# Optimization experiments

Measured on AMD Instinct MI355X. Metric: run time of the kernel, lower is better.

## Reference

```python
import jax, jax.numpy as jnp
import numpy as np

RADIUS = 1.3
RES = 256
N_INT = 128
STEP = 0.02


def grid_sample3d(grid, coords):
    # grid: [C, D, H, W]; coords: [N, 3] as (x, y, z) in [-1, 1]
    # trilinear, align_corners=True, border clamp (torch grid_sample semantics)
    D, H, W = grid.shape[1], grid.shape[2], grid.shape[3]

    def to_idx(c, size):
        return jnp.clip((c + 1.0) * 0.5 * (size - 1), 0.0, size - 1.0)

    x = to_idx(coords[:, 0], W)
    y = to_idx(coords[:, 1], H)
    z = to_idx(coords[:, 2], D)
    x0 = jnp.floor(x).astype(jnp.int32)
    y0 = jnp.floor(y).astype(jnp.int32)
    z0 = jnp.floor(z).astype(jnp.int32)
    x1 = jnp.minimum(x0 + 1, W - 1)
    y1 = jnp.minimum(y0 + 1, H - 1)
    z1 = jnp.minimum(z0 + 1, D - 1)
    wx = x - x0.astype(x.dtype)
    wy = y - y0.astype(y.dtype)
    wz = z - z0.astype(z.dtype)

    def g(zi, yi, xi):
        return grid[:, zi, yi, xi]  # [C, N]

    c00 = g(z0, y0, x0) * (1 - wx) + g(z0, y0, x1) * wx
    c01 = g(z0, y1, x0) * (1 - wx) + g(z0, y1, x1) * wx
    c10 = g(z1, y0, x0) * (1 - wx) + g(z1, y0, x1) * wx
    c11 = g(z1, y1, x0) * (1 - wx) + g(z1, y1, x1) * wx
    c0 = c00 * (1 - wy) + c01 * wy
    c1 = c10 * (1 - wy) + c11 * wy
    return (c0 * (1 - wz) + c1 * wz).T  # [N, C]


def sh16(d):
    # real spherical harmonics, degree 4 (instant-ngp / tcnn convention), d unit
    x, y, z = d[:, 0], d[:, 1], d[:, 2]
    xx, yy, zz = x * x, y * y, z * z
    xy, yz, xz = x * y, y * z, x * z
    return jnp.stack([
        jnp.full_like(x, 0.28209479177387814),
        -0.48860251190291987 * y,
        0.48860251190291987 * z,
        -0.48860251190291987 * x,
        1.0925484305920792 * xy,
        -1.0925484305920792 * yz,
        0.94617469575755997 * zz - 0.31539156525251999,
        -1.0925484305920792 * xz,
        0.54627421529603959 * (xx - yy),
        0.59004358992664352 * y * (-3.0 * xx + yy),
        2.8906114426405538 * xy * z,
        0.45704579946446572 * y * (1.0 - 5.0 * zz),
        0.3731763325901154 * z * (5.0 * zz - 3.0),
        0.45704579946446572 * x * (1.0 - 5.0 * zz),
        1.445305721320277 * z * (xx - yy),
        0.59004358992664352 * x * (-xx + 3.0 * yy),
    ], axis=-1)  # [N, 16]


def mlp3(x, W0, W1, W2):
    # FullyFusedMLP: no bias, ReLU hidden, linear output
    h = jnp.maximum(x @ W0, 0.0)
    h = jnp.maximum(h @ W1, 0.0)
    return h @ W2


def setup_inputs() -> dict:
    key = jax.random.key(0)
    k = jax.random.split(key, 10)
    B, FD, NF = 4096, 32, 16
    rays_o = jax.random.normal(k[0], (B, 3), jnp.float32) * 0.5
    rays_d = jax.random.normal(k[1], (B, 3), jnp.float32)
    G1 = jax.random.normal(k[2], (3, RES, RES, RES), jnp.float32) * 0.02
    F = jax.random.normal(k[3], (FD, NF, NF, NF), jnp.float32) * 0.05
    W_sig0 = jax.random.normal(k[4], (FD, 128), jnp.float32) / np.sqrt(FD).astype(np.float32)
    W_sig1 = jax.random.normal(k[5], (128, 128), jnp.float32) / np.float32(np.sqrt(128))
    W_sig2 = jax.random.normal(k[6], (128, 16), jnp.float32) / np.float32(np.sqrt(128))
    W_col0 = jax.random.normal(k[7], (31, 64), jnp.float32) / np.float32(np.sqrt(31))
    W_col1 = jax.random.normal(k[8], (64, 64), jnp.float32) / np.float32(np.sqrt(64))
    W_col2 = jax.random.normal(k[9], (64, 3), jnp.float32) / np.float32(np.sqrt(64))
    return {"rays_o": rays_o, "rays_d": rays_d, "G1": G1, "F": F,
            "W_sig0": W_sig0, "W_sig1": W_sig1, "W_sig2": W_sig2,
            "W_col0": W_col0, "W_col1": W_col1, "W_col2": W_col2}


def reference(rays_o, rays_d, G1, F, W_sig0, W_sig1, W_sig2, W_col0, W_col1, W_col2):
    B = rays_o.shape[0]
    d = rays_d / jnp.linalg.norm(rays_d, axis=-1, keepdims=True)
    # ray-sphere intersection |o + t d| = RADIUS (unit d)
    b = jnp.sum(rays_o * d, axis=-1)
    c = jnp.sum(rays_o * rays_o, axis=-1) - RADIUS ** 2
    disc = b * b - c
    hit = disc > 0
    s = jnp.sqrt(jnp.where(hit, disc, 1.0))
    tmin = jnp.where(hit, jnp.maximum(-b - s, 0.0), 0.0)
    tmax = jnp.where(hit, -b + s, 0.0)
    t = tmin[:, None] + jnp.arange(N_INT + 1, dtype=jnp.float32)[None, :] * STEP  # [B, n+1]
    tmid = 0.5 * (t[:, :-1] + t[:, 1:])  # [B, n]
    mask = hit[:, None] & (tmid <= tmax[:, None])  # [B, n]
    pts = rays_o[:, None, :] + d[:, None, :] * tmid[..., None]  # [B, n, 3]
    coords = (pts / RADIUS).reshape(-1, 3)  # in [-1, 1]
    # hash/indirection lookup: G1 gives learned coords into feature grid F
    g1 = grid_sample3d(G1, coords)        # [N, 3]
    feats = grid_sample3d(F, g1)          # [N, 32]
    sig_out = mlp3(feats, W_sig0, W_sig1, W_sig2)  # [N, 16]
    sigma = jnp.where(mask, sig_out[:, 0].reshape(B, N_INT), 0.0)
    sigma = jnp.maximum(sigma, 0.0)
    pd = jnp.broadcast_to(d[:, None, :], (B, N_INT, 3)).reshape(-1, 3)
    enc = sh16(pd)
    col_raw = mlp3(jnp.concatenate([enc, sig_out[:, 1:]], axis=-1), W_col0, W_col1, W_col2)
    col = jnp.where(mask[..., None], col_raw.reshape(B, N_INT, 3), 0.0)
    # volume rendering (sigma2alpha + shrgb2rgb with white background)
    alpha = 1.0 - jnp.exp(-sigma * STEP)
    T = jnp.cumprod(1.0 - alpha + 1e-10, axis=1)
    T_excl = jnp.concatenate([jnp.ones((B, 1), alpha.dtype), T[:, :-1]], axis=1)
    w = alpha * T_excl
    rgb = jnp.einsum('bn,bnc->bc', w, jax.nn.sigmoid(col))
    rgb = rgb + (1.0 - jnp.sum(w, axis=1, keepdims=True))
    return rgb
```

## Files before the change

kernel.cpp:

```cpp
#include <hip/hip_runtime.h>
#include <stdint.h>

#define STEP 0.02f
#define INV_RADIUS (1.0f/1.3f)
#define RADIUS 1.3f

typedef __bf16 bf16x8 __attribute__((ext_vector_type(8)));
typedef float  f32x4  __attribute__((ext_vector_type(4)));

#define FT_OFF   0
#define W0_OFF   262144
#define W1_OFF   270336
#define W2_OFF   303104
#define C0_OFF   307200
#define C1_OFF   311296
#define C2_OFF   319488

#define FE_OFF    0
#define HA_OFF    4096
#define HB_OFF    8192
#define CIN_OFF   12288
#define SIG_OFF   13312
#define COL_OFF   13824
#define WAVE_LDS  15872

__device__ __forceinline__ uint32_t pack2(float a, float b){
    uint32_t ua = __float_as_uint(a); ua += 0x7FFFu + ((ua>>16)&1u);
    uint32_t ub = __float_as_uint(b); ub += 0x7FFFu + ((ub>>16)&1u);
    return (ua>>16) | (ub & 0xFFFF0000u);
}
__device__ __forceinline__ unsigned short f2bf(float f){
    uint32_t u = __float_as_uint(f); u += 0x7FFFu + ((u>>16)&1u);
    return (unsigned short)(u>>16);
}
__device__ __forceinline__ void toidx(float c, float sizem1, int isize,
                                      int& i0, int& i1, float& w){
    float t = (c + 1.f) * 0.5f * sizem1;
    t = fminf(fmaxf(t, 0.f), sizem1);
    float f = floorf(t);
    i0 = (int)f;
    i1 = i0 + 1; if (i1 > isize - 1) i1 = isize - 1;
    w = t - f;
}
__device__ __forceinline__ void lds_fence(){
    asm volatile("s_waitcnt lgkmcnt(0)" ::: "memory");
}

__global__ __launch_bounds__(256) void prep_f(const float* __restrict__ F, uint32_t* __restrict__ ws){
    int idx = blockIdx.x * 256 + threadIdx.x;
    if (idx >= 4096) return;
    uint32_t out[16];
    #pragma unroll
    for (int c = 0; c < 16; c++){
        float a = F[(2*c  )*4096 + idx];
        float b = F[(2*c+1)*4096 + idx];
        out[c] = pack2(a, b);
    }
    uint4* dst = (uint4*)ws;
    #pragma unroll
    for (int q = 0; q < 4; q++)
        dst[idx*4 + q] = make_uint4(out[q*4], out[q*4+1], out[q*4+2], out[q*4+3]);
}

__global__ __launch_bounds__(256) void prep_w(const float* __restrict__ W0, const float* __restrict__ W1,
                                              const float* __restrict__ W2, const float* __restrict__ Wc0,
                                              const float* __restrict__ Wc1, const float* __restrict__ Wc2,
                                              char* __restrict__ ws){
    int gid = blockIdx.x * 256 + threadIdx.x;
    if (gid >= 58*64) return;
    int cg = gid >> 6, lane = gid & 63;
    const float* src; int K, N, base_cg, dstoff;
    if      (cg < 8)  { src = W0;  K = 32;  N = 128; base_cg = 0;  dstoff = W0_OFF; }
    else if (cg < 40) { src = W1;  K = 128; N = 128; base_cg = 8;  dstoff = W1_OFF; }
    else if (cg < 44) { src = W2;  K = 128; N = 16;  base_cg = 40; dstoff = W2_OFF; }
    else if (cg < 48) { src = Wc0; K = 31;  N = 64;  base_cg = 44; dstoff = C0_OFF; }
    else if (cg < 56) { src = Wc1; K = 64;  N = 64;  base_cg = 48; dstoff = C1_OFF; }
    else              { src = Wc2; K = 64;  N = 3;   base_cg = 56; dstoff = C2_OFF; }
    int local = cg - base_cg;
    int NT = (N + 15) >> 4;
    int nt = local % NT, kk = local / NT;
    int n = nt*16 + (lane & 15);
    int kbase = kk*32 + (lane >> 4)*8;
    uint32_t o[4];
    #pragma unroll
    for (int jj = 0; jj < 4; jj++){
        int k0 = kbase + jj*2, k1 = k0 + 1;
        float a = (n < N && k0 < K) ? src[k0*N + n] : 0.f;
        float b = (n < N && k1 < K) ? src[k1*N + n] : 0.f;
        o[jj] = pack2(a, b);
    }
    uint4* dst = (uint4*)(ws + dstoff);
    dst[local*64 + lane] = make_uint4(o[0], o[1], o[2], o[3]);
}

__global__ __launch_bounds__(256, 2)
void nerf_fused(const float* __restrict__ rays_o, const float* __restrict__ rays_d,
                const float* __restrict__ G1, const char* __restrict__ ws,
                float* __restrict__ out){
    __shared__ __align__(16) char smem[WAVE_LDS*4];
    const int tid  = threadIdx.x;
    const int wv   = tid >> 6;
    const int lane = tid & 63;
    const int nl   = lane & 15;
    const int quad = lane >> 4;
    const int ray  = blockIdx.x*4 + wv;
    char* WB = smem + wv*WAVE_LDS;

    float ox = rays_o[ray*3+0], oy = rays_o[ray*3+1], oz = rays_o[ray*3+2];
    float rx = rays_d[ray*3+0], ry = rays_d[ray*3+1], rz = rays_d[ray*3+2];
    float nrm = sqrtf(rx*rx + ry*ry + rz*rz);
    float dx = rx/nrm, dy = ry/nrm, dz = rz/nrm;
    float bq = ox*dx + oy*dy + oz*dz;
    float cq = ox*ox + oy*oy + oz*oz - RADIUS*RADIUS;
    float disc = bq*bq - cq;
    bool  hit = disc > 0.f;
    float sq   = sqrtf(hit ? disc : 1.f);
    float tmin = hit ? fmaxf(-bq - sq, 0.f) : 0.f;
    float tmax = hit ? (-bq + sq) : 0.f;

    {
        float X=dx, Y=dy, Z=dz;
        float xx=X*X, yy=Y*Y, zz=Z*Z, xy=X*Y, yz=Y*Z, xz=X*Z;
        float e[16];
        e[0]=0.28209479177387814f;
        e[1]=-0.48860251190291987f*Y;
        e[2]= 0.48860251190291987f*Z;
        e[3]=-0.48860251190291987f*X;
        e[4]= 1.0925484305920792f*xy;
        e[5]=-1.0925484305920792f*yz;
        e[6]= 0.94617469575756f*zz - 0.31539156525252f;
        e[7]=-1.0925484305920792f*xz;
        e[8]= 0.5462742152960396f*(xx-yy);
        e[9]= 0.5900435899266435f*Y*(-3.f*xx+yy);
        e[10]=2.890611442640554f*xy*Z;
        e[11]=0.4570457994644657f*Y*(1.f-5.f*zz);
        e[12]=0.3731763325901154f*Z*(5.f*zz-3.f);
        e[13]=0.4570457994644657f*X*(1.f-5.f*zz);
        e[14]=1.445305721320277f*Z*(xx-yy);
        e[15]=0.5900435899266435f*X*(-xx+3.f*yy);
        int rsw = (nl>>1)&3;
        if (quad < 2){
            uint4 v = make_uint4(pack2(e[quad*8+0], e[quad*8+1]),
                                 pack2(e[quad*8+2], e[quad*8+3]),
                                 pack2(e[quad*8+4], e[quad*8+5]),
                                 pack2(e[quad*8+6], e[quad*8+7]));
            *(uint4*)(WB + CIN_OFF + nl*64 + ((quad ^ rsw)*16)) = v;
        } else if (quad == 3){
            *(unsigned short*)(WB + CIN_OFF + nl*64 + ((3 ^ rsw)*16) + 14) = 0;
        }
    }

    const char* pW0 = ws + W0_OFF; const char* pW1 = ws + W1_OFF; const char* pW2 = ws + W2_OFF;
    const char* pC0 = ws + C0_OFF; const char* pC1 = ws + C1_OFF; const char* pC2 = ws + C2_OFF;
    const f32x4 vzero = {0.f, 0.f, 0.f, 0.f};
    float* SIGf = (float*)(WB + SIG_OFF);
    float* COLf = (float*)(WB + COL_OFF);

    #define RD_A(bp, linRow, m) \
        (*(const bf16x8*)((bp) + (linRow)*64 + ((quad ^ (((m)>>1)&3))*16)))
    #define LD_B(base, kk, NT, nt) \
        (*(const bf16x8*)((base) + (((kk)*(NT) + (nt))*64 + lane)*16))
    #define WR_H(bp, ROWS, m, kpos, val) \
        *(unsigned short*)((bp) + (((kpos)>>5)*(ROWS) + (m))*64 \
            + (((((kpos)>>3)&3) ^ (((m)>>1)&3))*16) + ((kpos)&7)*2) = f2bf(val)

    bf16x8 bW1[4][8];
    #pragma unroll
    for (int kk = 0; kk < 4; kk++)
        #pragma unroll
        for (int nt = 0; nt < 8; nt++)
            bW1[kk][nt] = LD_B(pW1, kk, 8, nt);
    bf16x8 bC1[2][4];
    #pragma unroll
    for (int kk = 0; kk < 2; kk++)
        #pragma unroll
        for (int nt = 0; nt < 4; nt++)
            bC1[kk][nt] = LD_B(pC1, kk, 4, nt);

    for (int half = 0; half < 2; half++){
        {
            int p = half*64 + lane;
            float tmid = tmin + ((float)p + 0.5f) * STEP;
            float px = (ox + dx*tmid) * INV_RADIUS;
            float py = (oy + dy*tmid) * INV_RADIUS;
            float pz = (oz + dz*tmid) * INV_RADIUS;
            int x0,x1,y0,y1,z0,z1; float wx,wy,wz;
            toidx(px, 255.f, 256, x0, x1, wx);
            toidx(py, 255.f, 256, y0, y1, wy);
            toidx(pz, 255.f, 256, z0, z1, wz);
            float g1v[3];
            #pragma unroll
            for (int ch = 0; ch < 3; ch++){
                const float* gp = G1 + ch*16777216;
                int b00 = (z0*256 + y0)*256, b01 = (z0*256 + y1)*256;
                int b10 = (z1*256 + y0)*256, b11 = (z1*256 + y1)*256;
                float c000 = gp[b00+x0], c001 = gp[b00+x1];
                float c010 = gp[b01+x0], c011 = gp[b01+x1];
                float c100 = gp[b10+x0], c101 = gp[b10+x1];
                float c110 = gp[b11+x0], c111 = gp[b11+x1];
                float c00 = c000 + (c001-c000)*wx;
                float c01 = c010 + (c011-c010)*wx;
                float c10 = c100 + (c101-c100)*wx;
                float c11 = c110 + (c111-c110)*wx;
                float c0 = c00 + (c01-c00)*wy;
                float c1 = c10 + (c11-c10)*wy;
                g1v[ch] = c0 + (c1-c0)*wz;
            }
            int fx0,fx1,fy0,fy1,fz0,fz1; float fwx,fwy,fwz;
            toidx(g1v[0], 15.f, 16, fx0, fx1, fwx);
            toidx(g1v[1], 15.f, 16, fy0, fy1, fwy);
            toidx(g1v[2], 15.f, 16, fz0, fz1, fwz);
            float feats[32];
            #pragma unroll
            for (int i = 0; i < 32; i++) feats[i] = 0.f;
            const uint4* Ft = (const uint4*)(ws + FT_OFF);
            #pragma unroll 2
            for (int corner = 0; corner < 8; corner++){
                int cz = (corner>>2)&1, cy = (corner>>1)&1, cx = corner&1;
                int xi = cx?fx1:fx0, yi = cy?fy1:fy0, zi = cz?fz1:fz0;
                float w = (cx?fwx:1.f-fwx) * (cy?fwy:1.f-fwy) * (cz?fwz:1.f-fwz);
                const uint4* cp = Ft + ((zi*16 + yi)*16 + xi)*4;
                #pragma unroll
                for (int q = 0; q < 4; q++){
                    uint4 v = cp[q];
                    uint32_t u[4] = {v.x, v.y, v.z, v.w};
                    #pragma unroll
                    for (int e = 0; e < 4; e++){
                        feats[q*8 + e*2    ] += w * __uint_as_float(u[e] << 16);
                        feats[q*8 + e*2 + 1] += w * __uint_as_float(u[e] & 0xFFFF0000u);
                    }
                }
            }
            int fsw = (lane>>1)&3;
            #pragma unroll
            for (int c = 0; c < 4; c++){
                uint4 v = make_uint4(pack2(feats[c*8+0], feats[c*8+1]),
                                     pack2(feats[c*8+2], feats[c*8+3]),
                                     pack2(feats[c*8+4], feats[c*8+5]),
                                     pack2(feats[c*8+6], feats[c*8+7]));
                *(uint4*)(WB + FE_OFF + lane*64 + ((c^fsw)*16)) = v;
            }
        }
        lds_fence();

        bf16x8 bW0[8];
        #pragma unroll
        for (int nt = 0; nt < 8; nt++) bW0[nt] = LD_B(pW0, 0, 8, nt);

        for (int mt = 0; mt < 4; mt++){
            const int mArow = mt*16 + nl;
            const int mW = quad*4;
            const int gRow = half*64 + mt*16 + mW;

            {
                bf16x8 a = RD_A(WB + FE_OFF, mArow, mArow);
                f32x4 acc[8];
                #pragma unroll
                for (int nt = 0; nt < 8; nt++)
                    acc[nt] = __builtin_amdgcn_mfma_f32_16x16x32_bf16(a, bW0[nt], vzero, 0, 0, 0);
                #pragma unroll
                for (int nt = 0; nt < 8; nt++)
                    #pragma unroll
                    for (int r = 0; r < 4; r++)
                        WR_H(WB + HA_OFF, 16, mW + r, nt*16 + nl, fmaxf(acc[nt][r], 0.f));
            }
            lds_fence();
            {
                f32x4 acc[8];
                #pragma unroll
                for (int nt = 0; nt < 8; nt++) acc[nt] = vzero;
                #pragma unroll
                for (int kk = 0; kk < 4; kk++){
                    bf16x8 a = RD_A(WB + HA_OFF, kk*16 + nl, nl);
                    #pragma unroll
                    for (int nt = 0; nt < 8; nt++)
                        acc[nt] = __builtin_amdgcn_mfma_f32_16x16x32_bf16(a, bW1[kk][nt], acc[nt], 0, 0, 0);
                }
                #pragma unroll
                for (int nt = 0; nt < 8; nt++)
                    #pragma unroll
                    for (int r = 0; r < 4; r++)
                        WR_H(WB + HB_OFF, 16, mW + r, nt*16 + nl, fmaxf(acc[nt][r], 0.f));
            }
            lds_fence();
            {
                f32x4 acc = vzero;
                #pragma unroll
                for (int kk = 0; kk < 4; kk++){
                    bf16x8 a = RD_A(WB + HB_OFF, kk*16 + nl, nl);
                    bf16x8 b = LD_B(pW2, kk, 1, 0);
                    acc = __builtin_amdgcn_mfma_f32_16x16x32_bf16(a, b, acc, 0, 0, 0);
                }
                #pragma unroll
                for (int r = 0; r < 4; r++){
                    float v = acc[r];
                    if (nl == 0) SIGf[gRow + r] = v;
                    else         WR_H(WB + CIN_OFF, 16, mW + r, 15 + nl, v);
                }
            }
            lds_fence();
            {
                bf16x8 a = RD_A(WB + CIN_OFF, nl, nl);
                f32x4 acc[4];
                #pragma unroll
                for (int nt = 0; nt < 4; nt++){
                    bf16x8 b = LD_B(pC0, 0, 4, nt);
                    acc[nt] = __builtin_amdgcn_mfma_f32_16x16x32_bf16(a, b, vzero, 0, 0, 0);
                }
                #pragma unroll
                for (int nt = 0; nt < 4; nt++)
                    #pragma unroll
                    for (int r = 0; r < 4; r++)
                        WR_H(WB + HA_OFF, 16, mW + r, nt*16 + nl, fmaxf(acc[nt][r], 0.f));
            }
            lds_fence();
            {
                f32x4 acc[4];
                #pragma unroll
                for (int nt = 0; nt < 4; nt++) acc[nt] = vzero;
                #pragma unroll
                for (int kk = 0; kk < 2; kk++){
                    bf16x8 a = RD_A(WB + HA_OFF, kk*16 + nl, nl);
                    #pragma unroll
                    for (int nt = 0; nt < 4; nt++)
                        acc[nt] = __builtin_amdgcn_mfma_f32_16x16x32_bf16(a, bC1[kk][nt], acc[nt], 0, 0, 0);
                }
                #pragma unroll
                for (int nt = 0; nt < 4; nt++)
                    #pragma unroll
                    for (int r = 0; r < 4; r++)
                        WR_H(WB + HB_OFF, 16, mW + r, nt*16 + nl, fmaxf(acc[nt][r], 0.f));
            }
            lds_fence();
            {
                f32x4 acc = vzero;
                #pragma unroll
                for (int kk = 0; kk < 2; kk++){
                    bf16x8 a = RD_A(WB + HB_OFF, kk*16 + nl, nl);
                    bf16x8 b = LD_B(pC2, kk, 1, 0);
                    acc = __builtin_amdgcn_mfma_f32_16x16x32_bf16(a, b, acc, 0, 0, 0);
                }
                #pragma unroll
                for (int r = 0; r < 4; r++)
                    if (nl < 3) COLf[(gRow + r)*4 + nl] = acc[r];
            }
            lds_fence();
        }
    }

    float t0 = tmin + ((float)lane + 0.5f) * STEP;
    float t1 = tmin + ((float)(lane + 64) + 0.5f) * STEP;
    bool  m0 = hit && (t0 <= tmax);
    bool  m1 = hit && (t1 <= tmax);
    float sig0 = m0 ? fmaxf(SIGf[lane], 0.f) : 0.f;
    float sig1 = m1 ? fmaxf(SIGf[lane + 64], 0.f) : 0.f;
    float e0 = expf(-sig0 * STEP), e1 = expf(-sig1 * STEP);
    float al0 = 1.f - e0, al1 = 1.f - e1;
    float li0 = logf(e0 + 1e-10f), li1 = logf(e1 + 1e-10f);
    float incl0 = li0, incl1 = li1;
    #pragma unroll
    for (int off = 1; off < 64; off <<= 1){
        float v0 = __shfl_up(incl0, off);
        float v1 = __shfl_up(incl1, off);
        if (lane >= off){ incl0 += v0; incl1 += v1; }
    }
    float tot0 = __shfl(incl0, 63);
    float ex0 = incl0 - li0;
    float ex1 = tot0 + incl1 - li1;
    float w0 = al0 * expf(ex0);
    float w1 = al1 * expf(ex1);
    float r = w0 / (1.f + expf(-COLf[lane*4+0])) + w1 / (1.f + expf(-COLf[(lane+64)*4+0]));
    float g = w0 / (1.f + expf(-COLf[lane*4+1])) + w1 / (1.f + expf(-COLf[(lane+64)*4+1]));
    float b = w0 / (1.f + expf(-COLf[lane*4+2])) + w1 / (1.f + expf(-COLf[(lane+64)*4+2]));
    float wa = w0 + w1;
    #pragma unroll
    for (int off = 32; off > 0; off >>= 1){
        r  += __shfl_xor(r,  off);
        g  += __shfl_xor(g,  off);
        b  += __shfl_xor(b,  off);
        wa += __shfl_xor(wa, off);
    }
    if (lane == 0){
        out[ray*3+0] = r + (1.f - wa);
        out[ray*3+1] = g + (1.f - wa);
        out[ray*3+2] = b + (1.f - wa);
    }
}

extern "C" void kernel_launch(void* const* d_in, const int* in_sizes, int n_in,
                              void* d_out, int out_size, void* d_ws, size_t ws_size,
                              hipStream_t stream){
    const float* rays_o = (const float*)d_in[0];
    const float* rays_d = (const float*)d_in[1];
    const float* G1     = (const float*)d_in[2];
    const float* F      = (const float*)d_in[3];
    prep_f<<<16, 256, 0, stream>>>(F, (uint32_t*)d_ws);
    prep_w<<<15, 256, 0, stream>>>((const float*)d_in[4], (const float*)d_in[5],
                                   (const float*)d_in[6], (const float*)d_in[7],
                                   (const float*)d_in[8], (const float*)d_in[9],
                                   (char*)d_ws);
    nerf_fused<<<1024, 256, 0, stream>>>(rays_o, rays_d, G1, (const char*)d_ws, (float*)d_out);
}
```

Before: 444.0 us.

## Keep MLP activations in registers via transposed MFMA and permlane swaps, skip masked samples

The MLP chain now computes transposed products (weights as the A operand), so each layer's output accumulators become the next layer's B fragment through bf16 packing and permlane16/32 swaps. This removes the LDS write/fence/read round trips between layers. The kernel also skips sample tiles beyond the ray's valid sample count and drops the register-resident W1/C1 weight caches in favour of per-use global loads. Blocks shrink to two waves with a smaller LDS footprint. The risks are extra global weight traffic and correctness hazards in the C0 input remap and permlane fragment assembly.

```diff
diff --git a/kernel.cpp b/kernel.cpp
--- a/kernel.cpp
+++ b/kernel.cpp
@@ -5,8 +5,9 @@
 #define INV_RADIUS (1.0f/1.3f)
 #define RADIUS 1.3f
 
-typedef __bf16 bf16x8 __attribute__((ext_vector_type(8)));
-typedef float  f32x4  __attribute__((ext_vector_type(4)));
+typedef __bf16   bf16x8 __attribute__((ext_vector_type(8)));
+typedef float    f32x4  __attribute__((ext_vector_type(4)));
+typedef uint32_t u32x4  __attribute__((ext_vector_type(4)));
 
 #define FT_OFF   0
 #define W0_OFF   262144
@@ -17,21 +18,14 @@
 #define C2_OFF   319488
 
 #define FE_OFF    0
-#define HA_OFF    4096
-#define HB_OFF    8192
-#define CIN_OFF   12288
-#define SIG_OFF   13312
-#define COL_OFF   13824
-#define WAVE_LDS  15872
+#define SIG_OFF   4096
+#define COL_OFF   4608
+#define WAVE_LDS  6656
 
 __device__ __forceinline__ uint32_t pack2(float a, float b){
     uint32_t ua = __float_as_uint(a); ua += 0x7FFFu + ((ua>>16)&1u);
     uint32_t ub = __float_as_uint(b); ub += 0x7FFFu + ((ub>>16)&1u);
     return (ua>>16) | (ub & 0xFFFF0000u);
-}
-__device__ __forceinline__ unsigned short f2bf(float f){
-    uint32_t u = __float_as_uint(f); u += 0x7FFFu + ((u>>16)&1u);
-    return (unsigned short)(u>>16);
 }
 __device__ __forceinline__ void toidx(float c, float sizem1, int isize,
                                       int& i0, int& i1, float& w){
@@ -45,21 +39,49 @@
 __device__ __forceinline__ void lds_fence(){
     asm volatile("s_waitcnt lgkmcnt(0)" ::: "memory");
 }
+__device__ __forceinline__ uint32_t cvtpk(float lo, float hi){
+    uint32_t r;
+    asm("v_cvt_pk_bf16_f32 %0, %1, %2" : "=v"(r) : "v"(lo), "v"(hi));
+    return r;
+}
+__device__ __forceinline__ void p32swap(uint32_t& a, uint32_t& b){
+    asm("v_permlane32_swap_b32 %0, %1" : "+v"(a), "+v"(b));
+}
+__device__ __forceinline__ void p16swap(uint32_t& a, uint32_t& b){
+    asm("v_permlane16_swap_b32 %0, %1" : "+v"(a), "+v"(b));
+}
+__device__ __forceinline__ uint32_t pkrelu(float a, float b){
+    return cvtpk(fmaxf(a, 0.f), fmaxf(b, 0.f));
+}
+__device__ __forceinline__ bf16x8 frag_from(uint32_t a, uint32_t b, uint32_t c, uint32_t d){
+    union { u32x4 u; bf16x8 h; } cv;
+    cv.u = (u32x4){a, b, c, d};
+    return cv.h;
+}
+__device__ __forceinline__ bf16x8 xpose4(const f32x4& t0, const f32x4& t1){
+    uint32_t A = pkrelu(t0[0], t0[1]);
+    uint32_t B = pkrelu(t0[2], t0[3]);
+    uint32_t C = pkrelu(t1[0], t1[1]);
+    uint32_t D = pkrelu(t1[2], t1[3]);
+    p32swap(A, C); p16swap(A, C);
+    p32swap(B, D); p16swap(B, D);
+    return frag_from(A, B, C, D);
+}
 
 __global__ __launch_bounds__(256) void prep_f(const float* __restrict__ F, uint32_t* __restrict__ ws){
     int idx = blockIdx.x * 256 + threadIdx.x;
     if (idx >= 4096) return;
-    uint32_t out[16];
+    uint32_t o[16];
     #pragma unroll
     for (int c = 0; c < 16; c++){
         float a = F[(2*c  )*4096 + idx];
         float b = F[(2*c+1)*4096 + idx];
-        out[c] = pack2(a, b);
+        o[c] = pack2(a, b);
     }
     uint4* dst = (uint4*)ws;
     #pragma unroll
     for (int q = 0; q < 4; q++)
-        dst[idx*4 + q] = make_uint4(out[q*4], out[q*4+1], out[q*4+2], out[q*4+3]);
+        dst[idx*4 + q] = make_uint4(o[q*4], o[q*4+1], o[q*4+2], o[q*4+3]);
 }
 
 __global__ __launch_bounds__(256) void prep_w(const float* __restrict__ W0, const float* __restrict__ W1,
@@ -76,6 +98,7 @@
     else if (cg < 48) { src = Wc0; K = 31;  N = 64;  base_cg = 44; dstoff = C0_OFF; }
     else if (cg < 56) { src = Wc1; K = 64;  N = 64;  base_cg = 48; dstoff = C1_OFF; }
     else              { src = Wc2; K = 64;  N = 3;   base_cg = 56; dstoff = C2_OFF; }
+    bool c0remap = (cg >= 44 && cg < 48);
     int local = cg - base_cg;
     int NT = (N + 15) >> 4;
     int nt = local % NT, kk = local / NT;
@@ -85,25 +108,29 @@
     #pragma unroll
     for (int jj = 0; jj < 4; jj++){
         int k0 = kbase + jj*2, k1 = k0 + 1;
-        float a = (n < N && k0 < K) ? src[k0*N + n] : 0.f;
-        float b = (n < N && k1 < K) ? src[k1*N + n] : 0.f;
+        int k0s = (c0remap && k0 > 16) ? k0 - 1 : k0;
+        int k1s = (c0remap && k1 > 16) ? k1 - 1 : k1;
+        bool v0 = (n < N) && (k0s < K) && !(c0remap && k0 == 16);
+        bool v1 = (n < N) && (k1s < K) && !(c0remap && k1 == 16);
+        float a = v0 ? src[k0s*N + n] : 0.f;
+        float b = v1 ? src[k1s*N + n] : 0.f;
         o[jj] = pack2(a, b);
     }
     uint4* dst = (uint4*)(ws + dstoff);
     dst[local*64 + lane] = make_uint4(o[0], o[1], o[2], o[3]);
 }
 
-__global__ __launch_bounds__(256, 2)
+__global__ __launch_bounds__(128, 3)
 void nerf_fused(const float* __restrict__ rays_o, const float* __restrict__ rays_d,
                 const float* __restrict__ G1, const char* __restrict__ ws,
                 float* __restrict__ out){
-    __shared__ __align__(16) char smem[WAVE_LDS*4];
+    __shared__ __align__(16) char smem[WAVE_LDS*2];
     const int tid  = threadIdx.x;
     const int wv   = tid >> 6;
     const int lane = tid & 63;
     const int nl   = lane & 15;
     const int quad = lane >> 4;
-    const int ray  = blockIdx.x*4 + wv;
+    const int ray  = blockIdx.x*2 + wv;
     char* WB = smem + wv*WAVE_LDS;
 
     float ox = rays_o[ray*3+0], oy = rays_o[ray*3+1], oz = rays_o[ray*3+2];
@@ -118,36 +145,31 @@
     float tmin = hit ? fmaxf(-bq - sq, 0.f) : 0.f;
     float tmax = hit ? (-bq + sq) : 0.f;
 
+    uint32_t encw0, encw1, encw2, encw3, cinmask;
     {
-        float X=dx, Y=dy, Z=dz;
-        float xx=X*X, yy=Y*Y, zz=Z*Z, xy=X*Y, yz=Y*Z, xz=X*Z;
-        float e[16];
-        e[0]=0.28209479177387814f;
-        e[1]=-0.48860251190291987f*Y;
-        e[2]= 0.48860251190291987f*Z;
-        e[3]=-0.48860251190291987f*X;
-        e[4]= 1.0925484305920792f*xy;
-        e[5]=-1.0925484305920792f*yz;
-        e[6]= 0.94617469575756f*zz - 0.31539156525252f;
-        e[7]=-1.0925484305920792f*xz;
-        e[8]= 0.5462742152960396f*(xx-yy);
-        e[9]= 0.5900435899266435f*Y*(-3.f*xx+yy);
-        e[10]=2.890611442640554f*xy*Z;
-        e[11]=0.4570457994644657f*Y*(1.f-5.f*zz);
-        e[12]=0.3731763325901154f*Z*(5.f*zz-3.f);
-        e[13]=0.4570457994644657f*X*(1.f-5.f*zz);
-        e[14]=1.445305721320277f*Z*(xx-yy);
-        e[15]=0.5900435899266435f*X*(-xx+3.f*yy);
-        int rsw = (nl>>1)&3;
-        if (quad < 2){
-            uint4 v = make_uint4(pack2(e[quad*8+0], e[quad*8+1]),
-                                 pack2(e[quad*8+2], e[quad*8+3]),
-                                 pack2(e[quad*8+4], e[quad*8+5]),
-                                 pack2(e[quad*8+6], e[quad*8+7]));
-            *(uint4*)(WB + CIN_OFF + nl*64 + ((quad ^ rsw)*16)) = v;
-        } else if (quad == 3){
-            *(unsigned short*)(WB + CIN_OFF + nl*64 + ((3 ^ rsw)*16) + 14) = 0;
-        }
+        float xx=dx*dx, yy=dy*dy, zz=dz*dz, xy=dx*dy, yz=dy*dz, xz=dx*dz;
+        float sh0 = 0.28209479177387814f;
+        float sh1 = -0.48860251190291987f*dy;
+        float sh2 =  0.48860251190291987f*dz;
+        float sh3 = -0.48860251190291987f*dx;
+        float sh4 =  1.0925484305920792f*xy;
+        float sh5 = -1.0925484305920792f*yz;
+        float sh6 =  0.94617469575756f*zz - 0.31539156525252f;
+        float sh7 = -1.0925484305920792f*xz;
+        float sh8 =  0.5462742152960396f*(xx-yy);
+        float sh9 =  0.5900435899266435f*dy*(-3.f*xx+yy);
+        float sh10 = 2.890611442640554f*xy*dz;
+        float sh11 = 0.4570457994644657f*dy*(1.f-5.f*zz);
+        float sh12 = 0.3731763325901154f*dz*(5.f*zz-3.f);
+        float sh13 = 0.4570457994644657f*dx*(1.f-5.f*zz);
+        float sh14 = 1.445305721320277f*dz*(xx-yy);
+        float sh15 = 0.5900435899266435f*dx*(-xx+3.f*yy);
+        bool q0 = (quad == 0);
+        encw0 = q0 ? pack2(sh0, sh1) : pack2(sh8,  sh9);
+        encw1 = q0 ? pack2(sh2, sh3) : pack2(sh10, sh11);
+        encw2 = q0 ? pack2(sh4, sh5) : pack2(sh12, sh13);
+        encw3 = q0 ? pack2(sh6, sh7) : pack2(sh14, sh15);
+        cinmask = (quad == 2) ? 0xFFFF0000u : 0xFFFFFFFFu;
     }
 
     const char* pW0 = ws + W0_OFF; const char* pW1 = ws + W1_OFF; const char* pW2 = ws + W2_OFF;
@@ -160,193 +182,168 @@
         (*(const bf16x8*)((bp) + (linRow)*64 + ((quad ^ (((m)>>1)&3))*16)))
     #define LD_B(base, kk, NT, nt) \
         (*(const bf16x8*)((base) + (((kk)*(NT) + (nt))*64 + lane)*16))
-    #define WR_H(bp, ROWS, m, kpos, val) \
-        *(unsigned short*)((bp) + (((kpos)>>5)*(ROWS) + (m))*64 \
-            + (((((kpos)>>3)&3) ^ (((m)>>1)&3))*16) + ((kpos)&7)*2) = f2bf(val)
-
-    bf16x8 bW1[4][8];
-    #pragma unroll
-    for (int kk = 0; kk < 4; kk++)
-        #pragma unroll
-        for (int nt = 0; nt < 8; nt++)
-            bW1[kk][nt] = LD_B(pW1, kk, 8, nt);
-    bf16x8 bC1[2][4];
-    #pragma unroll
-    for (int kk = 0; kk < 2; kk++)
-        #pragma unroll
-        for (int nt = 0; nt < 4; nt++)
-            bC1[kk][nt] = LD_B(pC1, kk, 4, nt);
-
-    for (int half = 0; half < 2; half++){
+
+    float Dn = (tmax - tmin) * (1.0f/STEP);
+    int nv = (int)fminf(128.f, fmaxf(0.f, floorf(Dn + 0.5f) + 1.f));
+    int nhalf = (nv > 64) ? 2 : 1;
+
+    for (int half = 0; half < nhalf; half++){
+        lds_fence();
         {
             int p = half*64 + lane;
-            float tmid = tmin + ((float)p + 0.5f) * STEP;
-            float px = (ox + dx*tmid) * INV_RADIUS;
-            float py = (oy + dy*tmid) * INV_RADIUS;
-            float pz = (oz + dz*tmid) * INV_RADIUS;
-            int x0,x1,y0,y1,z0,z1; float wx,wy,wz;
-            toidx(px, 255.f, 256, x0, x1, wx);
-            toidx(py, 255.f, 256, y0, y1, wy);
-            toidx(pz, 255.f, 256, z0, z1, wz);
-            float g1v[3];
-            #pragma unroll
-            for (int ch = 0; ch < 3; ch++){
-                const float* gp = G1 + ch*16777216;
-                int b00 = (z0*256 + y0)*256, b01 = (z0*256 + y1)*256;
-                int b10 = (z1*256 + y0)*256, b11 = (z1*256 + y1)*256;
-                float c000 = gp[b00+x0], c001 = gp[b00+x1];
-                float c010 = gp[b01+x0], c011 = gp[b01+x1];
-                float c100 = gp[b10+x0], c101 = gp[b10+x1];
-                float c110 = gp[b11+x0], c111 = gp[b11+x1];
-                float c00 = c000 + (c001-c000)*wx;
-                float c01 = c010 + (c011-c010)*wx;
-                float c10 = c100 + (c101-c100)*wx;
-                float c11 = c110 + (c111-c110)*wx;
-                float c0 = c00 + (c01-c00)*wy;
-                float c1 = c10 + (c11-c10)*wy;
-                g1v[ch] = c0 + (c1-c0)*wz;
-            }
-            int fx0,fx1,fy0,fy1,fz0,fz1; float fwx,fwy,fwz;
-            toidx(g1v[0], 15.f, 16, fx0, fx1, fwx);
-            toidx(g1v[1], 15.f, 16, fy0, fy1, fwy);
-            toidx(g1v[2], 15.f, 16, fz0, fz1, fwz);
-            float feats[32];
-            #pragma unroll
-            for (int i = 0; i < 32; i++) feats[i] = 0.f;
-            const uint4* Ft = (const uint4*)(ws + FT_OFF);
-            #pragma unroll 2
-            for (int corner = 0; corner < 8; corner++){
-                int cz = (corner>>2)&1, cy = (corner>>1)&1, cx = corner&1;
-                int xi = cx?fx1:fx0, yi = cy?fy1:fy0, zi = cz?fz1:fz0;
-                float w = (cx?fwx:1.f-fwx) * (cy?fwy:1.f-fwy) * (cz?fwz:1.f-fwz);
-                const uint4* cp = Ft + ((zi*16 + yi)*16 + xi)*4;
+            if (p < nv){
+                float tmid = tmin + ((float)p + 0.5f) * STEP;
+                float px = (ox + dx*tmid) * INV_RADIUS;
+                float py = (oy + dy*tmid) * INV_RADIUS;
+                float pz = (oz + dz*tmid) * INV_RADIUS;
+                int x0,x1,y0,y1,z0,z1; float wx,wy,wz;
+                toidx(px, 255.f, 256, x0, x1, wx);
+                toidx(py, 255.f, 256, y0, y1, wy);
+                toidx(pz, 255.f, 256, z0, z1, wz);
+                float g1v[3];
                 #pragma unroll
-                for (int q = 0; q < 4; q++){
-                    uint4 v = cp[q];
-                    uint32_t u[4] = {v.x, v.y, v.z, v.w};
+                for (int ch = 0; ch < 3; ch++){
+                    const float* gp = G1 + ch*16777216;
+                    int b00 = (z0*256 + y0)*256, b01 = (z0*256 + y1)*256;
+                    int b10 = (z1*256 + y0)*256, b11 = (z1*256 + y1)*256;
+                    float c000 = gp[b00+x0], c001 = gp[b00+x1];
+                    float c010 = gp[b01+x0], c011 = gp[b01+x1];
+                    float c100 = gp[b10+x0], c101 = gp[b10+x1];
+                    float c110 = gp[b11+x0], c111 = gp[b11+x1];
+                    float c00 = c000 + (c001-c000)*wx;
+                    float c01 = c010 + (c011-c010)*wx;
+                    float c10 = c100 + (c101-c100)*wx;
+                    float c11 = c110 + (c111-c110)*wx;
+                    float c0 = c00 + (c01-c00)*wy;
+                    float c1 = c10 + (c11-c10)*wy;
+                    g1v[ch] = c0 + (c1-c0)*wz;
+                }
+                int fx0,fx1,fy0,fy1,fz0,fz1; float fwx,fwy,fwz;
+                toidx(g1v[0], 15.f, 16, fx0, fx1, fwx);
+                toidx(g1v[1], 15.f, 16, fy0, fy1, fwy);
+                toidx(g1v[2], 15.f, 16, fz0, fz1, fwz);
+                float feats[32];
+                #pragma unroll
+                for (int i = 0; i < 32; i++) feats[i] = 0.f;
+                const uint4* Ft = (const uint4*)(ws + FT_OFF);
+                #pragma unroll 2
+                for (int corner = 0; corner < 8; corner++){
+                    int cz = (corner>>2)&1, cy = (corner>>1)&1, cx = corner&1;
+                    int xi = cx?fx1:fx0, yi = cy?fy1:fy0, zi = cz?fz1:fz0;
+                    float w = (cx?fwx:1.f-fwx) * (cy?fwy:1.f-fwy) * (cz?fwz:1.f-fwz);
+                    const uint4* cp = Ft + ((zi*16 + yi)*16 + xi)*4;
                     #pragma unroll
-                    for (int e = 0; e < 4; e++){
-                        feats[q*8 + e*2    ] += w * __uint_as_float(u[e] << 16);
-                        feats[q*8 + e*2 + 1] += w * __uint_as_float(u[e] & 0xFFFF0000u);
+                    for (int q = 0; q < 4; q++){
+                        uint4 v = cp[q];
+                        uint32_t u[4] = {v.x, v.y, v.z, v.w};
+                        #pragma unroll
+                        for (int e = 0; e < 4; e++){
+                            feats[q*8 + e*2    ] += w * __uint_as_float(u[e] << 16);
+                            feats[q*8 + e*2 + 1] += w * __uint_as_float(u[e] & 0xFFFF0000u);
+                        }
                     }
                 }
-            }
-            int fsw = (lane>>1)&3;
-            #pragma unroll
-            for (int c = 0; c < 4; c++){
-                uint4 v = make_uint4(pack2(feats[c*8+0], feats[c*8+1]),
-                                     pack2(feats[c*8+2], feats[c*8+3]),
-                                     pack2(feats[c*8+4], feats[c*8+5]),
-                                     pack2(feats[c*8+6], feats[c*8+7]));
-                *(uint4*)(WB + FE_OFF + lane*64 + ((c^fsw)*16)) = v;
+                int fsw = (lane>>1)&3;
+                #pragma unroll
+                for (int c = 0; c < 4; c++){
+                    uint4 v = make_uint4(pack2(feats[c*8+0], feats[c*8+1]),
+                                         pack2(feats[c*8+2], feats[c*8+3]),
+                                         pack2(feats[c*8+4], feats[c*8+5]),
+                                         pack2(feats[c*8+6], feats[c*8+7]));
+                    *(uint4*)(WB + FE_OFF + lane*64 + ((c^fsw)*16)) = v;
+                }
             }
         }
         lds_fence();
 
-        bf16x8 bW0[8];
+        bf16x8 bW2[4], bC0[4], bC2[2];
         #pragma unroll
-        for (int nt = 0; nt < 8; nt++) bW0[nt] = LD_B(pW0, 0, 8, nt);
-
-        for (int mt = 0; mt < 4; mt++){
+        for (int kk = 0; kk < 4; kk++) bW2[kk] = LD_B(pW2, kk, 1, 0);
+        #pragma unroll
+        for (int nt = 0; nt < 4; nt++) bC0[nt] = LD_B(pC0, 0, 4, nt);
+        #pragma unroll
+        for (int kk = 0; kk < 2; kk++) bC2[kk] = LD_B(pC2, kk, 1, 0);
+
+        int rem = nv - half*64;
+        int mtmax = (rem >= 64) ? 4 : ((rem + 15) >> 4);
+        #pragma unroll 1
+        for (int mt = 0; mt < mtmax; mt++){
             const int mArow = mt*16 + nl;
-            const int mW = quad*4;
-            const int gRow = half*64 + mt*16 + mW;
-
-            {
-                bf16x8 a = RD_A(WB + FE_OFF, mArow, mArow);
-                f32x4 acc[8];
+            const int tb = half*64 + mt*16;
+
+            bf16x8 fe = RD_A(WB + FE_OFF, mArow, mArow);
+            f32x4 a0[8];
+            #pragma unroll
+            for (int nt = 0; nt < 8; nt++)
+                a0[nt] = __builtin_amdgcn_mfma_f32_16x16x32_bf16(LD_B(pW0,0,8,nt), fe, vzero, 0,0,0);
+            bf16x8 h1[4];
+            #pragma unroll
+            for (int kk = 0; kk < 4; kk++)
+                h1[kk] = xpose4(a0[2*kk], a0[2*kk+1]);
+
+            f32x4 a1[8];
+            #pragma unroll
+            for (int nt = 0; nt < 8; nt++) a1[nt] = vzero;
+            #pragma unroll
+            for (int kk = 0; kk < 4; kk++)
                 #pragma unroll
                 for (int nt = 0; nt < 8; nt++)
-                    acc[nt] = __builtin_amdgcn_mfma_f32_16x16x32_bf16(a, bW0[nt], vzero, 0, 0, 0);
-                #pragma unroll
-                for (int nt = 0; nt < 8; nt++)
-                    #pragma unroll
-                    for (int r = 0; r < 4; r++)
-                        WR_H(WB + HA_OFF, 16, mW + r, nt*16 + nl, fmaxf(acc[nt][r], 0.f));
-            }
-            lds_fence();
-            {
-                f32x4 acc[8];
-                #pragma unroll
-                for (int nt = 0; nt < 8; nt++) acc[nt] = vzero;
-                #pragma unroll
-                for (int kk = 0; kk < 4; kk++){
-                    bf16x8 a = RD_A(WB + HA_OFF, kk*16 + nl, nl);
-                    #pragma unroll
-                    for (int nt = 0; nt < 8; nt++)
-                        acc[nt] = __builtin_amdgcn_mfma_f32_16x16x32_bf16(a, bW1[kk][nt], acc[nt], 0, 0, 0);
-                }
-                #pragma unroll
-                for (int nt = 0; nt < 8; nt++)
-                    #pragma unroll
-                    for (int r = 0; r < 4; r++)
-                        WR_H(WB + HB_OFF, 16, mW + r, nt*16 + nl, fmaxf(acc[nt][r], 0.f));
-            }
-            lds_fence();
-            {
-                f32x4 acc = vzero;
-                #pragma unroll
-                for (int kk = 0; kk < 4; kk++){
-                    bf16x8 a = RD_A(WB + HB_OFF, kk*16 + nl, nl);
-                    bf16x8 b = LD_B(pW2, kk, 1, 0);
-                    acc = __builtin_amdgcn_mfma_f32_16x16x32_bf16(a, b, acc, 0, 0, 0);
-                }
-                #pragma unroll
-                for (int r = 0; r < 4; r++){
-                    float v = acc[r];
-                    if (nl == 0) SIGf[gRow + r] = v;
-                    else         WR_H(WB + CIN_OFF, 16, mW + r, 15 + nl, v);
-                }
-            }
-            lds_fence();
-            {
-                bf16x8 a = RD_A(WB + CIN_OFF, nl, nl);
-                f32x4 acc[4];
-                #pragma unroll
-                for (int nt = 0; nt < 4; nt++){
-                    bf16x8 b = LD_B(pC0, 0, 4, nt);
-                    acc[nt] = __builtin_amdgcn_mfma_f32_16x16x32_bf16(a, b, vzero, 0, 0, 0);
-                }
+                    a1[nt] = __builtin_amdgcn_mfma_f32_16x16x32_bf16(LD_B(pW1,kk,8,nt), h1[kk], a1[nt], 0,0,0);
+            bf16x8 h2[4];
+            #pragma unroll
+            for (int kk = 0; kk < 4; kk++)
+                h2[kk] = xpose4(a1[2*kk], a1[2*kk+1]);
+
+            f32x4 sacc = vzero;
+            #pragma unroll
+            for (int kk = 0; kk < 4; kk++)
+                sacc = __builtin_amdgcn_mfma_f32_16x16x32_bf16(bW2[kk], h2[kk], sacc, 0,0,0);
+            if (quad == 0) SIGf[tb + nl] = sacc[0];
+
+            uint32_t ca = cvtpk(sacc[0], sacc[1]);
+            uint32_t cb = cvtpk(sacc[2], sacc[3]);
+            p32swap(ca, cb); p16swap(ca, cb);
+            uint32_t cw0 = encw0, cw2 = encw2;
+            p32swap(cw0, ca);
+            p32swap(cw2, cb);
+            cw0 &= cinmask;
+            uint32_t cw1 = (quad < 2) ? encw1 : ca;
+            uint32_t cw3 = (quad < 2) ? encw3 : cb;
+            bf16x8 cin = frag_from(cw0, cw1, cw2, cw3);
+
+            f32x4 c0[4];
+            #pragma unroll
+            for (int nt = 0; nt < 4; nt++)
+                c0[nt] = __builtin_amdgcn_mfma_f32_16x16x32_bf16(bC0[nt], cin, vzero, 0,0,0);
+            bf16x8 g1[2];
+            #pragma unroll
+            for (int kk = 0; kk < 2; kk++)
+                g1[kk] = xpose4(c0[2*kk], c0[2*kk+1]);
+
+            f32x4 c1[4];
+            #pragma unroll
+            for (int nt = 0; nt < 4; nt++) c1[nt] = vzero;
+            #pragma unroll
+            for (int kk = 0; kk < 2; kk++)
                 #pragma unroll
                 for (int nt = 0; nt < 4; nt++)
-                    #pragma unroll
-                    for (int r = 0; r < 4; r++)
-                        WR_H(WB + HA_OFF, 16, mW + r, nt*16 + nl, fmaxf(acc[nt][r], 0.f));
+                    c1[nt] = __builtin_amdgcn_mfma_f32_16x16x32_bf16(LD_B(pC1,kk,4,nt), g1[kk], c1[nt], 0,0,0);
+            bf16x8 g2[2];
+            #pragma unroll
+            for (int kk = 0; kk < 2; kk++)
+                g2[kk] = xpose4(c1[2*kk], c1[2*kk+1]);
+
+            f32x4 cc = vzero;
+            #pragma unroll
+            for (int kk = 0; kk < 2; kk++)
+                cc = __builtin_amdgcn_mfma_f32_16x16x32_bf16(bC2[kk], g2[kk], cc, 0,0,0);
+            if (quad == 0){
+                *(float2*)(COLf + (tb + nl)*4) = make_float2(cc[0], cc[1]);
+                COLf[(tb + nl)*4 + 2] = cc[2];
             }
-            lds_fence();
-            {
-                f32x4 acc[4];
-                #pragma unroll
-                for (int nt = 0; nt < 4; nt++) acc[nt] = vzero;
-                #pragma unroll
-                for (int kk = 0; kk < 2; kk++){
-                    bf16x8 a = RD_A(WB + HA_OFF, kk*16 + nl, nl);
-                    #pragma unroll
-                    for (int nt = 0; nt < 4; nt++)
-                        acc[nt] = __builtin_amdgcn_mfma_f32_16x16x32_bf16(a, bC1[kk][nt], acc[nt], 0, 0, 0);
-                }
-                #pragma unroll
-                for (int nt = 0; nt < 4; nt++)
-                    #pragma unroll
-                    for (int r = 0; r < 4; r++)
-                        WR_H(WB + HB_OFF, 16, mW + r, nt*16 + nl, fmaxf(acc[nt][r], 0.f));
-            }
-            lds_fence();
-            {
-                f32x4 acc = vzero;
-                #pragma unroll
-                for (int kk = 0; kk < 2; kk++){
-                    bf16x8 a = RD_A(WB + HB_OFF, kk*16 + nl, nl);
-                    bf16x8 b = LD_B(pC2, kk, 1, 0);
-                    acc = __builtin_amdgcn_mfma_f32_16x16x32_bf16(a, b, acc, 0, 0, 0);
-                }
-                #pragma unroll
-                for (int r = 0; r < 4; r++)
-                    if (nl < 3) COLf[(gRow + r)*4 + nl] = acc[r];
-            }
-            lds_fence();
         }
     }
+    lds_fence();
 
     float t0 = tmin + ((float)lane + 0.5f) * STEP;
     float t1 = tmin + ((float)(lane + 64) + 0.5f) * STEP;
@@ -369,9 +366,15 @@
     float ex1 = tot0 + incl1 - li1;
     float w0 = al0 * expf(ex0);
     float w1 = al1 * expf(ex1);
-    float r = w0 / (1.f + expf(-COLf[lane*4+0])) + w1 / (1.f + expf(-COLf[(lane+64)*4+0]));
-    float g = w0 / (1.f + expf(-COLf[lane*4+1])) + w1 / (1.f + expf(-COLf[(lane+64)*4+1]));
-    float b = w0 / (1.f + expf(-COLf[lane*4+2])) + w1 / (1.f + expf(-COLf[(lane+64)*4+2]));
+    float cr0 = m0 ? COLf[lane*4+0] : 0.f;
+    float cg0 = m0 ? COLf[lane*4+1] : 0.f;
+    float cb0 = m0 ? COLf[lane*4+2] : 0.f;
+    float cr1 = m1 ? COLf[(lane+64)*4+0] : 0.f;
+    float cg1 = m1 ? COLf[(lane+64)*4+1] : 0.f;
+    float cb1 = m1 ? COLf[(lane+64)*4+2] : 0.f;
+    float r = w0 / (1.f + expf(-cr0)) + w1 / (1.f + expf(-cr1));
+    float g = w0 / (1.f + expf(-cg0)) + w1 / (1.f + expf(-cg1));
+    float b = w0 / (1.f + expf(-cb0)) + w1 / (1.f + expf(-cb1));
     float wa = w0 + w1;
     #pragma unroll
     for (int off = 32; off > 0; off >>= 1){
@@ -385,6 +388,8 @@
         out[ray*3+1] = g + (1.f - wa);
         out[ray*3+2] = b + (1.f - wa);
     }
+    #undef RD_A
+    #undef LD_B
 }
 
 extern "C" void kernel_launch(void* const* d_in, const int* in_sizes, int n_in,
@@ -399,5 +404,5 @@
                                    (const float*)d_in[6], (const float*)d_in[7],
                                    (const float*)d_in[8], (const float*)d_in[9],
                                    (char*)d_ws);
-    nerf_fused<<<1024, 256, 0, stream>>>(rays_o, rays_d, G1, (const char*)d_ws, (float*)d_out);
-}
+    nerf_fused<<<2048, 128, 0, stream>>>(rays_o, rays_d, G1, (const char*)d_ws, (float*)d_out);
+}
```

Result: faster. 428.6 us (-3.5%).
